# Optimization experiments

Measured on AMD Instinct MI355X. Metric: run time of the kernel, lower is better.

## Reference

```python
import jax, jax.numpy as jnp
import numpy as np

B, N, K = 4096, 64, 4


def _jump_sum(Ls, rho):
    # sum_k L_k @ rho @ L_k^dagger  (real dtype -> dagger == transpose)
    return jnp.einsum('kij,bjl,kml->bim', Ls, rho, Ls)


def _sandwich(U, rho):
    # U @ rho @ U^dagger
    return jnp.einsum('ij,bjl,ml->bim', U, rho, U)


def setup_inputs() -> dict:
    key = jax.random.key(0)
    k = jax.random.split(key, 6)
    eye = jnp.eye(N, dtype=jnp.float32)
    rho0 = jax.random.normal(k[0], (B, N, N), dtype=jnp.float32)
    # propagators: near-identity perturbations, Um well-conditioned for the LU solve
    U1 = eye + 0.1 * jax.random.normal(k[1], (N, N), dtype=jnp.float32)
    Um = eye + 0.1 * jax.random.normal(k[2], (N, N), dtype=jnp.float32)
    Ls0 = jax.random.normal(k[3], (K, N, N), dtype=jnp.float32)
    Lsmid = jax.random.normal(k[4], (K, N, N), dtype=jnp.float32)
    Ls1 = jax.random.normal(k[5], (K, N, N), dtype=jnp.float32)
    dt = jnp.asarray(0.01, dtype=jnp.float32)
    return {'rho0': rho0, 'U1': U1, 'Um': Um, 'Ls0': Ls0,
            'Lsmid': Lsmid, 'Ls1': Ls1, 'dt': dt}


def reference(rho0, U1, Um, Ls0, Lsmid, Ls1, dt):
    # propagator from t+dt/2 to t+dt via LU solve: solve(Um^T, U1^T)^T
    Um1 = jnp.linalg.solve(Um.T, U1.T).T

    # stage 1
    rho1 = rho0
    # stage 2 (SecondStage, no_jump_0 = Um, Ls = Ls0, aii = 0.5)
    rho2 = _sandwich(Um, rho0 + 0.5 * dt * _jump_sum(Ls0, rho1))
    # stage 3 (SameTimeStage, no_jump_0 = Um, Ls = Lsmid, aii = 0.5)
    rho3 = _sandwich(Um, rho0) + 0.5 * dt * _jump_sum(Lsmid, rho2)
    rho23 = rho2 + rho3
    # stage 4 (RKStage, no_jump_0 = U1, no_jump_i = Um1, Ls = Lsmid, aii = 1.0)
    rho4 = _sandwich(U1, rho0) + _sandwich(Um1, dt * _jump_sum(Lsmid, rho3))

    out = (_sandwich(U1, rho0 + (dt / 6) * _jump_sum(Ls0, rho1))
           + _sandwich(Um1, (dt / 3) * _jump_sum(Lsmid, rho23))
           + (dt / 6) * _jump_sum(Ls1, rho4))
    return out
```

## Files before the change

kernel.cpp:

```cpp
#include <hip/hip_runtime.h>


typedef __attribute__((ext_vector_type(16))) float f32x16;
typedef __attribute__((ext_vector_type(8))) __bf16 bf16x8;

#define MATB 8192

__device__ __forceinline__ unsigned short bf16rne(float x) {
  unsigned u = __builtin_bit_cast(unsigned, x);
  return (unsigned short)((u + 0x7FFFu + ((u >> 16) & 1u)) >> 16);
}
__device__ __forceinline__ float bflo(unsigned u) {
  return __builtin_bit_cast(float, u << 16);
}
__device__ __forceinline__ float bfhi(unsigned u) {
  return __builtin_bit_cast(float, u & 0xFFFF0000u);
}

__device__ __forceinline__ void mm4_gl(f32x16& acc, const char* __restrict__ gP,
                                       const char* ldsQ, int vq, int lh) {
#pragma unroll
  for (int s = 0; s < 4; ++s) {
    bf16x8 a = *(const bf16x8*)(gP + s * 1024);
    bf16x8 b = *(const bf16x8*)(ldsQ + (((2 * s + lh) ^ vq) << 4));
    acc = __builtin_amdgcn_mfma_f32_32x32x16_bf16(a, b, acc, 0, 0, 0);
  }
}
__device__ __forceinline__ void mm4_lg(f32x16& acc, const char* ldsP, int vp,
                                       int lh, const char* __restrict__ gQ) {
#pragma unroll
  for (int s = 0; s < 4; ++s) {
    bf16x8 a = *(const bf16x8*)(ldsP + (((2 * s + lh) ^ vp) << 4));
    bf16x8 b = *(const bf16x8*)(gQ + s * 1024);
    acc = __builtin_amdgcn_mfma_f32_32x32x16_bf16(a, b, acc, 0, 0, 0);
  }
}

__device__ __forceinline__ void wtile(char* base, int ti, int slotc, int coff,
                                      int lh, const f32x16& v) {
#pragma unroll
  for (int r = 0; r < 16; ++r) {
    int row = ti * 32 + 4 * lh + (r & 3) + 8 * (r >> 2);
    int ps = (slotc ^ ((4 * ti + (r >> 2)) & 7)) << 4;
    *(unsigned short*)(base + row * 128 + ps + coff) = bf16rne(v[r]);
  }
}
__device__ __forceinline__ void wtile_rmw(char* base, int ti, int slotc, int coff,
                                          int lh, const f32x16& v, float s) {
#pragma unroll
  for (int r = 0; r < 16; ++r) {
    int row = ti * 32 + 4 * lh + (r & 3) + 8 * (r >> 2);
    int ps = (slotc ^ ((4 * ti + (r >> 2)) & 7)) << 4;
    unsigned short* p = (unsigned short*)(base + row * 128 + ps + coff);
    float old = bflo((unsigned)*p);
    *p = bf16rne(old + s * v[r]);
  }
}

__device__ __forceinline__ void axpy(char* D, const char* A, float s,
                                     const char* B, int tid) {
#pragma unroll
  for (int j = 0; j < 8; ++j) {
    int off = (tid + 256 * j) * 4;
    unsigned a = *(const unsigned*)(A + off);
    unsigned b = *(const unsigned*)(B + off);
    float lo = bflo(a) + s * bflo(b);
    float hi = bfhi(a) + s * bfhi(b);
    *(unsigned*)(D + off) = (unsigned)bf16rne(lo) | ((unsigned)bf16rne(hi) << 16);
  }
}

__global__ __launch_bounds__(256) void kraus_invert(
    const float* __restrict__ U1, const float* __restrict__ Um,
    float* __restrict__ Um1) {
  __shared__ float M[64][66];
  __shared__ float X[64][66];
  int tid = threadIdx.x;
#pragma unroll
  for (int it = 0; it < 16; ++it) {
    int idx = tid + 256 * it;
    int r = idx >> 6, c = idx & 63;
    M[r][c] = Um[idx];
    X[r][c] = (r == c) ? 1.0f : 0.0f;
  }
  __syncthreads();
  for (int k = 0; k < 64; ++k) {
    if (tid < 64) {
      float ip = 1.0f / M[k][k];
      M[k][tid] *= ip;
      X[k][tid] *= ip;
    }
    __syncthreads();
    int r = tid & 63, q = tid >> 6;
    float f = M[r][k];
    __syncthreads();
    if (r != k) {
#pragma unroll
      for (int cc = 0; cc < 16; ++cc) {
        int c = q * 16 + cc;
        M[r][c] -= f * M[k][c];
        X[r][c] -= f * X[k][c];
      }
    }
    __syncthreads();
  }
  for (int it = 0; it < 16; ++it) {
    int idx = tid + 256 * it;
    int i = idx >> 6, j = idx & 63;
    float s = 0.0f;
#pragma unroll 4
    for (int k = 0; k < 64; ++k) s += U1[i * 64 + k] * X[k][j];
    Um1[idx] = s;
  }
}

__global__ __launch_bounds__(256) void kraus_prepack(
    const float* __restrict__ U1, const float* __restrict__ Um,
    const float* __restrict__ Ls0, const float* __restrict__ Lsmid,
    const float* __restrict__ Ls1, float* __restrict__ ws) {
  const float* Um1 = ws;
  unsigned short* dst = (unsigned short*)((char*)ws + 16384);
  int o = blockIdx.x;
  const float* s;
  if (o == 0) s = U1;
  else if (o == 1) s = Um;
  else if (o == 2) s = Um1;
  else if (o < 7) s = Ls0 + (o - 3) * 4096;
  else if (o < 11) s = Lsmid + (o - 7) * 4096;
  else s = Ls1 + (o - 11) * 4096;
  unsigned short* d = dst + o * 4096;
  int tid = threadIdx.x;
#pragma unroll
  for (int j = 0; j < 16; ++j) {
    int idx = tid + 256 * j;
    int f = idx >> 9, l = (idx >> 3) & 63, i = idx & 7;
    int t = f >> 2, ss = f & 3;
    int R = t * 32 + (l & 31);
    int C = ss * 16 + (l >> 5) * 8 + i;
    d[idx] = bf16rne(s[R * 64 + C]);
  }
}

__global__ __launch_bounds__(256, 4) void kraus_main(
    const float* __restrict__ rho0g, const float* __restrict__ dtp,
    const char* __restrict__ gfrag, float* __restrict__ outg) {
  __shared__ __align__(16) char lds[5 * MATB];
  char* B0 = lds;
  char* B1 = B0 + MATB;
  char* B3 = B1 + MATB;
  char* B4 = B3 + MATB;
  char* TMP = B4 + MATB;

  const int tid = threadIdx.x;
  const int l = tid & 63, w = tid >> 6;
  const int ti = w >> 1, tj = w & 1;
  const int l31 = l & 31, lh = l >> 5;
  const int vA = (4 * ti + (l31 >> 3)) & 7;
  const int vB = (4 * tj + (l31 >> 3)) & 7;
  const int rA = (ti * 32 + l31) * 128;
  const int rB = (tj * 32 + l31) * 128;
  const int slotc = 4 * tj + (l31 >> 3), coff = (l31 & 7) * 2;
  const float dt = dtp[0];
  const size_t b = blockIdx.x;
  const char* gA0 = gfrag + ti * 4096 + l * 16;
  const char* gB0 = gfrag + tj * 4096 + l * 16;

  auto GL = [&](f32x16& acc, int op, const char* q) {
    mm4_gl(acc, gA0 + op * 8192, q + rB, vB, lh);
  };
  auto LG = [&](f32x16& acc, const char* p, int op) {
    mm4_lg(acc, p + rA, vA, lh, gB0 + op * 8192);
  };
  auto WT = [&](char* dst, const f32x16& v) { wtile(dst, ti, slotc, coff, lh, v); };

  {
    const float* src = rho0g + b * 4096 + tid * 16;
    float vals[16];
#pragma unroll
    for (int q = 0; q < 4; ++q) {
      float4 f = *(const float4*)(src + q * 4);
      vals[q * 4 + 0] = f.x; vals[q * 4 + 1] = f.y;
      vals[q * 4 + 2] = f.z; vals[q * 4 + 3] = f.w;
    }
    int r = tid >> 2, c0 = (tid & 3) * 16;
    int sr = r >> 3, cr = (r & 7) * 2;
#pragma unroll
    for (int u = 0; u < 16; ++u) {
      int row = c0 + u;
      int ps = (sr ^ ((row >> 3) & 7)) << 4;
      *(unsigned short*)(B0 + row * 128 + ps + cr) = bf16rne(vals[u]);
    }
  }
  __syncthreads();

  f32x16 outacc = {};

  {
    f32x16 J = {};
    { f32x16 t = {}; GL(t, 3, B0); WT(TMP, t); } __syncthreads();
    { f32x16 t = {}; GL(J, 3, TMP); GL(t, 4, B0); WT(B1, t); } __syncthreads();
    { f32x16 t = {}; GL(J, 4, B1); GL(t, 5, B0); WT(TMP, t); } __syncthreads();
    { f32x16 t = {}; GL(J, 5, TMP); GL(t, 6, B0); WT(B1, t); } __syncthreads();
    { GL(J, 6, B1); WT(TMP, J); } __syncthreads();
  }

  { f32x16 t = {}; GL(t, 0, TMP); WT(B1, t); axpy(B4, B0, 0.5f * dt, TMP, tid); }
  __syncthreads();

  { f32x16 s = {}; LG(s, B1, 0); outacc += (dt / 6.f) * s;
    f32x16 t = {}; GL(t, 0, B0); WT(TMP, t); }
  __syncthreads();

  { f32x16 s = {}; LG(s, TMP, 0); outacc += s;
    f32x16 p = {}; GL(p, 0, TMP); WT(B1, p);
    f32x16 t = {}; GL(t, 1, B4); WT(B3, t); }
  __syncthreads();

  { f32x16 r2 = {}; GL(r2, 1, B3); WT(B4, r2);
    f32x16 t = {}; GL(t, 1, B0); WT(TMP, t); }
  __syncthreads();

  { f32x16 s = {}; GL(s, 1, TMP); WT(B0, s);
    f32x16 t = {}; GL(t, 7, B4); WT(B3, t); }
  __syncthreads();

  {
    f32x16 J = {};
    { f32x16 t = {}; GL(J, 7, B3); GL(t, 8, B4); WT(TMP, t); } __syncthreads();
    { f32x16 t = {}; GL(J, 8, TMP); GL(t, 9, B4); WT(B3, t); } __syncthreads();
    { f32x16 t = {}; GL(J, 9, B3); GL(t, 10, B4); WT(TMP, t); } __syncthreads();
    { GL(J, 10, TMP); WT(B4, J); } __syncthreads();
  }

  axpy(B0, B0, 0.5f * dt, B4, tid);
  __syncthreads();

  {
    f32x16 J = {};
    { f32x16 t = {}; GL(t, 7, B0); WT(TMP, t); } __syncthreads();
    { f32x16 t = {}; GL(J, 7, TMP); GL(t, 8, B0); WT(B3, t); } __syncthreads();
    { f32x16 t = {}; GL(J, 8, B3); GL(t, 9, B0); WT(TMP, t); } __syncthreads();
    { f32x16 t = {}; GL(J, 9, TMP); GL(t, 10, B0); WT(B3, t); } __syncthreads();
    { GL(J, 10, B3); WT(TMP, J); } __syncthreads();
  }

  { f32x16 a = {}; GL(a, 2, TMP); f32x16 c = a; GL(c, 2, B4);
    WT(B0, a); WT(B3, c); }
  __syncthreads();

  { f32x16 s = {}; LG(s, B3, 2); outacc += (dt / 3.f) * s;
    f32x16 q = {}; GL(q, 2, B0); wtile_rmw(B1, ti, slotc, coff, lh, q, dt); }
  __syncthreads();

  {
    f32x16 J = {};
    { f32x16 t = {}; GL(t, 11, B1); WT(TMP, t); } __syncthreads();
    { f32x16 t = {}; LG(J, TMP, 11); GL(t, 12, B1); WT(B4, t); } __syncthreads();
    { f32x16 t = {}; LG(J, B4, 12); GL(t, 13, B1); WT(TMP, t); } __syncthreads();
    { f32x16 t = {}; LG(J, TMP, 13); GL(t, 14, B1); WT(B4, t); } __syncthreads();
    { LG(J, B4, 14); outacc += (dt / 6.f) * J; }
  }

  {
    float* op = outg + b * 4096 + (size_t)(ti * 32 + lh * 4) * 64 + tj * 32 + l31;
#pragma unroll
    for (int r = 0; r < 16; ++r) {
      int row = (r & 3) + 8 * (r >> 2);
      op[row * 64] = outacc[r];
    }
  }
}

extern "C" void kernel_launch(void* const* d_in, const int* in_sizes, int n_in,
                              void* d_out, int out_size, void* d_ws, size_t ws_size,
                              hipStream_t stream) {
  const float* rho0 = (const float*)d_in[0];
  const float* U1 = (const float*)d_in[1];
  const float* Um = (const float*)d_in[2];
  const float* Ls0 = (const float*)d_in[3];
  const float* Lsmid = (const float*)d_in[4];
  const float* Ls1 = (const float*)d_in[5];
  const float* dtp = (const float*)d_in[6];
  float* out = (float*)d_out;
  float* ws = (float*)d_ws;

  const int B = in_sizes[0] >> 12;

  kraus_invert<<<1, 256, 0, stream>>>(U1, Um, ws);
  kraus_prepack<<<15, 256, 0, stream>>>(U1, Um, Ls0, Lsmid, Ls1, ws);
  kraus_main<<<B, 256, 0, stream>>>(rho0, dtp, (const char*)d_ws + 16384, out);
}
```

Measured before the change: 233.8 us.

## Keep sandwich intermediates in registers via lane shuffles instead of LDS round-trips

Each sandwich product X·A·B is restructured so each wave computes the full 64-wide intermediate row panel (two 32x32 tiles) in registers. It then feeds that panel as the MFMA operand through bf16 packing and cross-half lane shuffles, instead of writing it to shared memory and synchronizing. This removes most __syncthreads and LDS temp writes and shrinks LDS from five to four buffers. In exchange each wave redundantly computes the first product for both column blocks, which doubles first-stage MFMA work. Launch bounds drop to two blocks per SM to allow the extra register pressure.

```diff
diff --git a/kernel.cpp b/kernel.cpp
--- a/kernel.cpp
+++ b/kernel.cpp
@@ -16,16 +16,27 @@
 __device__ __forceinline__ float bfhi(unsigned u) {
   return __builtin_bit_cast(float, u & 0xFFFF0000u);
 }
-
-__device__ __forceinline__ void mm4_gl(f32x16& acc, const char* __restrict__ gP,
-                                       const char* ldsQ, int vq, int lh) {
-#pragma unroll
-  for (int s = 0; s < 4; ++s) {
-    bf16x8 a = *(const bf16x8*)(gP + s * 1024);
-    bf16x8 b = *(const bf16x8*)(ldsQ + (((2 * s + lh) ^ vq) << 4));
-    acc = __builtin_amdgcn_mfma_f32_32x32x16_bf16(a, b, acc, 0, 0, 0);
-  }
-}
+__device__ __forceinline__ unsigned pk2(float lo, float hi) {
+  return (unsigned)bf16rne(lo) | ((unsigned)bf16rne(hi) << 16);
+}
+
+union U4 { uint4 u; bf16x8 h; };
+
+__device__ __forceinline__ bf16x8 assemble(const f32x16& t, int b8, int lh) {
+  unsigned u0 = pk2(t[b8 + 0], t[b8 + 1]);
+  unsigned u1 = pk2(t[b8 + 2], t[b8 + 3]);
+  unsigned w0 = pk2(t[b8 + 4], t[b8 + 5]);
+  unsigned w1 = pk2(t[b8 + 6], t[b8 + 7]);
+  unsigned su0 = __shfl_xor(u0, 32);
+  unsigned su1 = __shfl_xor(u1, 32);
+  unsigned sw0 = __shfl_xor(w0, 32);
+  unsigned sw1 = __shfl_xor(w1, 32);
+  U4 r;
+  r.u = make_uint4(lh ? sw0 : u0, lh ? sw1 : u1,
+                   lh ? w0 : su0, lh ? w1 : su1);
+  return r.h;
+}
+
 __device__ __forceinline__ void mm4_lg(f32x16& acc, const char* ldsP, int vp,
                                        int lh, const char* __restrict__ gQ) {
 #pragma unroll
@@ -33,6 +44,27 @@
     bf16x8 a = *(const bf16x8*)(ldsP + (((2 * s + lh) ^ vp) << 4));
     bf16x8 b = *(const bf16x8*)(gQ + s * 1024);
     acc = __builtin_amdgcn_mfma_f32_32x32x16_bf16(a, b, acc, 0, 0, 0);
+  }
+}
+
+__device__ __forceinline__ void secondGP(f32x16& acc, const char* __restrict__ gP,
+                                         const f32x16& t0, const f32x16& t1,
+                                         int lh) {
+#pragma unroll
+  for (int s = 0; s < 4; ++s) {
+    bf16x8 q = assemble((s < 2) ? t0 : t1, (s & 1) * 8, lh);
+    bf16x8 p = *(const bf16x8*)(gP + s * 1024);
+    acc = __builtin_amdgcn_mfma_f32_32x32x16_bf16(p, q, acc, 0, 0, 0);
+  }
+}
+__device__ __forceinline__ void secondGQ(f32x16& acc, const f32x16& t0,
+                                         const f32x16& t1,
+                                         const char* __restrict__ gQ, int lh) {
+#pragma unroll
+  for (int s = 0; s < 4; ++s) {
+    bf16x8 p = assemble((s < 2) ? t0 : t1, (s & 1) * 8, lh);
+    bf16x8 q = *(const bf16x8*)(gQ + s * 1024);
+    acc = __builtin_amdgcn_mfma_f32_32x32x16_bf16(p, q, acc, 0, 0, 0);
   }
 }
 
@@ -141,35 +173,43 @@
   }
 }
 
-__global__ __launch_bounds__(256, 4) void kraus_main(
+__global__ __launch_bounds__(256, 2) void kraus_main(
     const float* __restrict__ rho0g, const float* __restrict__ dtp,
     const char* __restrict__ gfrag, float* __restrict__ outg) {
-  __shared__ __align__(16) char lds[5 * MATB];
-  char* B0 = lds;
-  char* B1 = B0 + MATB;
-  char* B3 = B1 + MATB;
-  char* B4 = B3 + MATB;
-  char* TMP = B4 + MATB;
+  __shared__ __align__(16) char lds[4 * MATB];
+  char* S0 = lds;
+  char* S1 = S0 + MATB;
+  char* S2 = S1 + MATB;
+  char* S3 = S2 + MATB;
 
   const int tid = threadIdx.x;
   const int l = tid & 63, w = tid >> 6;
   const int ti = w >> 1, tj = w & 1;
   const int l31 = l & 31, lh = l >> 5;
-  const int vA = (4 * ti + (l31 >> 3)) & 7;
-  const int vB = (4 * tj + (l31 >> 3)) & 7;
-  const int rA = (ti * 32 + l31) * 128;
-  const int rB = (tj * 32 + l31) * 128;
+  const int row0 = l31 * 128;
+  const int row1 = (32 + l31) * 128;
+  const int vk0 = l31 >> 3;
+  const int vk1 = 4 + (l31 >> 3);
   const int slotc = 4 * tj + (l31 >> 3), coff = (l31 & 7) * 2;
   const float dt = dtp[0];
   const size_t b = blockIdx.x;
-  const char* gA0 = gfrag + ti * 4096 + l * 16;
-  const char* gB0 = gfrag + tj * 4096 + l * 16;
-
-  auto GL = [&](f32x16& acc, int op, const char* q) {
-    mm4_gl(acc, gA0 + op * 8192, q + rB, vB, lh);
+
+  auto GF = [&](int op, int blk) {
+    return gfrag + op * 8192 + blk * 4096 + l * 16;
   };
-  auto LG = [&](f32x16& acc, const char* p, int op) {
-    mm4_lg(acc, p + rA, vA, lh, gB0 + op * 8192);
+  auto firsts = [&](const char* X, int op, int blk, f32x16& t0, f32x16& t1) {
+    mm4_lg(t0, X + row0, vk0, lh, GF(op, blk));
+    mm4_lg(t1, X + row1, vk1, lh, GF(op, blk));
+  };
+  auto sandPlain = [&](f32x16& acc, const char* X, int op1, int op2) {
+    f32x16 t0 = {}, t1 = {};
+    firsts(X, op1, ti, t0, t1);
+    secondGQ(acc, t0, t1, GF(op2, tj), lh);
+  };
+  auto sandHat = [&](f32x16& acc, const char* X, int op1, int op2) {
+    f32x16 t0 = {}, t1 = {};
+    firsts(X, op1, tj, t0, t1);
+    secondGP(acc, GF(op2, ti), t0, t1, lh);
   };
   auto WT = [&](char* dst, const f32x16& v) { wtile(dst, ti, slotc, coff, lh, v); };
 
@@ -188,7 +228,7 @@
     for (int u = 0; u < 16; ++u) {
       int row = c0 + u;
       int ps = (sr ^ ((row >> 3) & 7)) << 4;
-      *(unsigned short*)(B0 + row * 128 + ps + cr) = bf16rne(vals[u]);
+      *(unsigned short*)(S0 + row * 128 + ps + cr) = bf16rne(vals[u]);
     }
   }
   __syncthreads();
@@ -197,68 +237,66 @@
 
   {
     f32x16 J = {};
-    { f32x16 t = {}; GL(t, 3, B0); WT(TMP, t); } __syncthreads();
-    { f32x16 t = {}; GL(J, 3, TMP); GL(t, 4, B0); WT(B1, t); } __syncthreads();
-    { f32x16 t = {}; GL(J, 4, B1); GL(t, 5, B0); WT(TMP, t); } __syncthreads();
-    { f32x16 t = {}; GL(J, 5, TMP); GL(t, 6, B0); WT(B1, t); } __syncthreads();
-    { GL(J, 6, B1); WT(TMP, J); } __syncthreads();
-  }
-
-  { f32x16 t = {}; GL(t, 0, TMP); WT(B1, t); axpy(B4, B0, 0.5f * dt, TMP, tid); }
-  __syncthreads();
-
-  { f32x16 s = {}; LG(s, B1, 0); outacc += (dt / 6.f) * s;
-    f32x16 t = {}; GL(t, 0, B0); WT(TMP, t); }
-  __syncthreads();
-
-  { f32x16 s = {}; LG(s, TMP, 0); outacc += s;
-    f32x16 p = {}; GL(p, 0, TMP); WT(B1, p);
-    f32x16 t = {}; GL(t, 1, B4); WT(B3, t); }
-  __syncthreads();
-
-  { f32x16 r2 = {}; GL(r2, 1, B3); WT(B4, r2);
-    f32x16 t = {}; GL(t, 1, B0); WT(TMP, t); }
-  __syncthreads();
-
-  { f32x16 s = {}; GL(s, 1, TMP); WT(B0, s);
-    f32x16 t = {}; GL(t, 7, B4); WT(B3, t); }
+#pragma unroll
+    for (int k = 0; k < 4; ++k) sandHat(J, S0, 3 + k, 3 + k);
+    WT(S1, J);
+  }
+  __syncthreads();
+
+  {
+    f32x16 a = {};
+    sandPlain(a, S1, 0, 0);
+    outacc += (dt / 6.f) * a;
+    axpy(S2, S0, 0.5f * dt, S1, tid);
+  }
+  __syncthreads();
+
+  {
+    { f32x16 a = {}; sandPlain(a, S0, 0, 0); outacc += a; }
+    { f32x16 a = {}; sandHat(a, S0, 0, 0); WT(S1, a); }
+    { f32x16 a = {}; sandHat(a, S2, 1, 1); WT(S3, a); }
+  }
+  __syncthreads();
+
+  {
+    f32x16 a = {};
+    sandHat(a, S0, 1, 1);
+    WT(S2, a);
+  }
   __syncthreads();
 
   {
     f32x16 J = {};
-    { f32x16 t = {}; GL(J, 7, B3); GL(t, 8, B4); WT(TMP, t); } __syncthreads();
-    { f32x16 t = {}; GL(J, 8, TMP); GL(t, 9, B4); WT(B3, t); } __syncthreads();
-    { f32x16 t = {}; GL(J, 9, B3); GL(t, 10, B4); WT(TMP, t); } __syncthreads();
-    { GL(J, 10, TMP); WT(B4, J); } __syncthreads();
-  }
-
-  axpy(B0, B0, 0.5f * dt, B4, tid);
+#pragma unroll
+    for (int k = 0; k < 4; ++k) sandHat(J, S3, 7 + k, 7 + k);
+    WT(S0, J);
+  }
+  __syncthreads();
+
+  axpy(S3, S2, 0.5f * dt, S0, tid);
   __syncthreads();
 
   {
     f32x16 J = {};
-    { f32x16 t = {}; GL(t, 7, B0); WT(TMP, t); } __syncthreads();
-    { f32x16 t = {}; GL(J, 7, TMP); GL(t, 8, B0); WT(B3, t); } __syncthreads();
-    { f32x16 t = {}; GL(J, 8, B3); GL(t, 9, B0); WT(TMP, t); } __syncthreads();
-    { f32x16 t = {}; GL(J, 9, TMP); GL(t, 10, B0); WT(B3, t); } __syncthreads();
-    { GL(J, 10, B3); WT(TMP, J); } __syncthreads();
-  }
-
-  { f32x16 a = {}; GL(a, 2, TMP); f32x16 c = a; GL(c, 2, B4);
-    WT(B0, a); WT(B3, c); }
-  __syncthreads();
-
-  { f32x16 s = {}; LG(s, B3, 2); outacc += (dt / 3.f) * s;
-    f32x16 q = {}; GL(q, 2, B0); wtile_rmw(B1, ti, slotc, coff, lh, q, dt); }
+#pragma unroll
+    for (int k = 0; k < 4; ++k) sandHat(J, S3, 7 + k, 7 + k);
+    WT(S2, J);
+  }
+  __syncthreads();
+
+  {
+    { f32x16 a = {}; sandPlain(a, S0, 2, 2); outacc += (dt / 3.f) * a; }
+    { f32x16 a = {}; sandPlain(a, S2, 2, 2); outacc += (dt / 3.f) * a; }
+    { f32x16 a = {}; sandHat(a, S2, 2, 2);
+      wtile_rmw(S1, ti, slotc, coff, lh, a, dt); }
+  }
   __syncthreads();
 
   {
     f32x16 J = {};
-    { f32x16 t = {}; GL(t, 11, B1); WT(TMP, t); } __syncthreads();
-    { f32x16 t = {}; LG(J, TMP, 11); GL(t, 12, B1); WT(B4, t); } __syncthreads();
-    { f32x16 t = {}; LG(J, B4, 12); GL(t, 13, B1); WT(TMP, t); } __syncthreads();
-    { f32x16 t = {}; LG(J, TMP, 13); GL(t, 14, B1); WT(B4, t); } __syncthreads();
-    { LG(J, B4, 14); outacc += (dt / 6.f) * J; }
+#pragma unroll
+    for (int k = 0; k < 4; ++k) sandPlain(J, S1, 11 + k, 11 + k);
+    outacc += (dt / 6.f) * J;
   }
 
   {
```

Result: slower. 283.2 us (+21.1%).
